# Kernel optimization log

Measured on AMD Instinct MI355X. Metric: run time of the kernel, lower is better.

Reference implementation:

```python
import jax, jax.numpy as jnp
import numpy as np

N_FEATURES = 128
N_ACTIONS = 16
HIDDEN = 256
BATCH = 4096
IN_DIM = N_FEATURES + N_ACTIONS  # 144


def setup_inputs() -> dict:
    key = jax.random.key(0)
    k1, k2, k3, k4 = jax.random.split(key, 4)
    f_t = jax.random.normal(k1, (BATCH, N_FEATURES), dtype=jnp.float32)
    a_t = jax.random.normal(k2, (BATCH, N_ACTIONS), dtype=jnp.float32)
    # Stacked per-feature MLP params (one small MLP per output feature).
    W1 = jax.random.normal(k3, (N_FEATURES, IN_DIM, HIDDEN), dtype=jnp.float32) / np.sqrt(IN_DIM)
    b1 = jnp.zeros((N_FEATURES, HIDDEN), dtype=jnp.float32)
    W2 = jax.random.normal(k4, (N_FEATURES, HIDDEN), dtype=jnp.float32) / np.sqrt(HIDDEN)
    b2 = jnp.zeros((N_FEATURES,), dtype=jnp.float32)
    return {"f_t": f_t, "a_t": a_t, "W1": W1, "b1": b1, "W2": W2, "b2": b2}


def reference(f_t, a_t, W1, b1, W2, b2):
    # fa_t: [B, F+A] shared input to all per-feature models
    fa_t = jnp.concatenate((f_t, a_t), axis=1)
    # Grouped GEMM replacing parallel_apply over n_features tiny MLPs:
    # h: [M, B, H]
    h = jax.nn.relu(jnp.einsum('bi,mih->mbh', fa_t, W1) + b1[:, None, :])
    # out: [B, M]  (each model emits a single scalar per example)
    out = jnp.einsum('mbh,mh->bm', h, W2) + b2[None, :]
    # skip_connection=True, additional=False, all=False -> add f_t
    return out + f_t
```

## Files before the change

### kernel.cpp

```cpp
#include <hip/hip_runtime.h>
#include <hip/hip_bf16.h>

#define BATCH   4096
#define NF      128
#define NA      16
#define IN_DIM  144
#define KP      160
#define KF      192
#define HID     256

typedef __attribute__((ext_vector_type(8))) short bf16x8;
typedef __attribute__((ext_vector_type(4))) float f32x4;
typedef unsigned int u32;

__device__ __forceinline__ void gl_lds16(const void* gsrc, void* ldst) {
    __builtin_amdgcn_global_load_lds(
        (const __attribute__((address_space(1))) u32*)gsrc,
        (__attribute__((address_space(3))) u32*)ldst, 16, 0, 0);
}

__global__ void convert_all(const float* __restrict__ W1,
                            const float* __restrict__ b1,
                            const float* __restrict__ f_t,
                            const float* __restrict__ a_t,
                            __hip_bfloat16* __restrict__ w1t,
                            __hip_bfloat16* __restrict__ fab) {
    const int bid = blockIdx.x;
    const int t = threadIdx.x;
    if (bid < 1280) {
        __shared__ float tile[16][HID];
        int m = bid / 10;
        int kc = bid - m * 10;
        int k0 = kc * 16;
        if (kc < 9) {
#pragma unroll
            for (int i = 0; i < 16; ++i)
                tile[i][t] = W1[((size_t)m * IN_DIM + (k0 + i)) * HID + t];
            __syncthreads();
            union { ushort us[16]; uint4 q[2]; } pk;
#pragma unroll
            for (int i = 0; i < 16; ++i) {
                __hip_bfloat16 h = __float2bfloat16(tile[i][t]);
                pk.us[i] = *(ushort*)&h;
            }
            uint4* dst = (uint4*)(w1t + ((size_t)m * HID + t) * KP + k0);
            dst[0] = pk.q[0];
            dst[1] = pk.q[1];
        } else {
            union { ushort us[8]; uint4 q; } pk;
#pragma unroll
            for (int j = 0; j < 8; ++j) pk.us[j] = 0;
            __hip_bfloat16 hb = __float2bfloat16(b1[(size_t)m * HID + t]);
            pk.us[0] = *(ushort*)&hb;
            uint4 z = {0u, 0u, 0u, 0u};
            uint4* dst = (uint4*)(w1t + ((size_t)m * HID + t) * KP + IN_DIM);
            dst[0] = pk.q;
            dst[1] = z;
        }
    } else {
        int c = (bid - 1280) * 256 + t;
        const int total = BATCH * (KF / 8);
        if (c >= total) return;
        int row = c / 24;
        int cc = c - row * 24;
        union { ushort us[8]; uint4 q; } pk;
#pragma unroll
        for (int j = 0; j < 8; ++j) {
            int k = cc * 8 + j;
            float v;
            if (k < NF)            v = f_t[(size_t)row * NF + k];
            else if (k < IN_DIM)   v = a_t[(size_t)row * NA + (k - NF)];
            else if (k == IN_DIM)  v = 1.0f;
            else                   v = 0.0f;
            __hip_bfloat16 h = __float2bfloat16(v);
            pk.us[j] = *(ushort*)&h;
        }
        int pc = cc ^ (row & 7);
        *(uint4*)(fab + (size_t)row * KF + pc * 8) = pk.q;
    }
}

__global__ __launch_bounds__(256, 3) void fused_mlp(
        const __hip_bfloat16* __restrict__ fab,
        const __hip_bfloat16* __restrict__ w1t,
        const float* __restrict__ W2,
        const float* __restrict__ b2,
        const float* __restrict__ f_t,
        float* __restrict__ out) {
    __shared__ __align__(16) __hip_bfloat16 Abuf[2][32 * KF];
    __shared__ __align__(16) float partial[2][4][32];

    const int bid = blockIdx.x;
    const int m     = bid & 127;
    const int slice = bid >> 7;
    const int row_base = slice * 512;
    const int t = threadIdx.x;
    const int w = t >> 6;
    const int lane = t & 63;
    const int lrow = lane & 15;
    const int g = lane >> 4;
    const int xr = (lrow & 7) << 4;

    bf16x8 bfrag[4][5];
#pragma unroll
    for (int hi = 0; hi < 4; ++hi) {
        const int col = w * 64 + hi * 16 + lrow;
        const __hip_bfloat16* wp = w1t + ((size_t)m * HID + col) * KP + g * 8;
#pragma unroll
        for (int ks = 0; ks < 5; ++ks)
            bfrag[hi][ks] = *(const bf16x8*)(wp + ks * 32);
    }
    f32x4 w2v[4];
#pragma unroll
    for (int hi = 0; hi < 4; ++hi)
        w2v[hi] = *(const f32x4*)(W2 + (size_t)m * HID + w * 64 + hi * 16 + g * 4);
    const float b2v = b2[m];
    const f32x4 zc = (f32x4){0.f, 0.f, 0.f, 0.f};

    {
        const char* src = (const char*)(fab + (size_t)row_base * KF);
        char* dst = (char*)&Abuf[0][0];
#pragma unroll
        for (int i = 0; i < 3; ++i)
            gl_lds16(src + (size_t)(t + i * 256) * 16, dst + (t + i * 256) * 16);
    }
    __syncthreads();

    for (int tile = 0; tile < 16; ++tile) {
        const int cur = tile & 1;
        const int r0 = row_base + tile * 32;

        if (tile < 15) {
            const char* src = (const char*)(fab + (size_t)(r0 + 32) * KF);
            char* dst = (char*)&Abuf[cur ^ 1][0];
#pragma unroll
            for (int i = 0; i < 3; ++i)
                gl_lds16(src + (size_t)(t + i * 256) * 16, dst + (t + i * 256) * 16);
        }
        float skipv = 0.0f;
        if (t < 32) skipv = f_t[(size_t)(r0 + t) * NF + m];

        f32x4 acc[4][2];
        const char* ab = (const char*)&Abuf[cur][0];

        {
            bf16x8 a[2];
#pragma unroll
            for (int bj = 0; bj < 2; ++bj) {
                int off = (bj * 16 + lrow) * 384 + ((g * 16) ^ xr);
                a[bj] = *(const bf16x8*)(ab + off);
            }
#pragma unroll
            for (int hi = 0; hi < 4; ++hi)
#pragma unroll
                for (int bj = 0; bj < 2; ++bj)
                    acc[hi][bj] = __builtin_amdgcn_mfma_f32_16x16x32_bf16(
                        bfrag[hi][0], a[bj], zc, 0, 0, 0);
        }
#pragma unroll
        for (int ks = 1; ks < 5; ++ks) {
            bf16x8 a[2];
#pragma unroll
            for (int bj = 0; bj < 2; ++bj) {
                int off = (bj * 16 + lrow) * 384 + ((ks * 64 + g * 16) ^ xr);
                a[bj] = *(const bf16x8*)(ab + off);
            }
#pragma unroll
            for (int hi = 0; hi < 4; ++hi)
#pragma unroll
                for (int bj = 0; bj < 2; ++bj)
                    acc[hi][bj] = __builtin_amdgcn_mfma_f32_16x16x32_bf16(
                        bfrag[hi][ks], a[bj], acc[hi][bj], 0, 0, 0);
        }

        float sarr[2];
#pragma unroll
        for (int bj = 0; bj < 2; ++bj) {
            float sr0 = 0.f, sr1 = 0.f, sr2 = 0.f, sr3 = 0.f;
#pragma unroll
            for (int hi = 0; hi < 4; ++hi) {
                float h0 = acc[hi][bj][0]; h0 = h0 > 0.f ? h0 : 0.f;
                float h1 = acc[hi][bj][1]; h1 = h1 > 0.f ? h1 : 0.f;
                float h2 = acc[hi][bj][2]; h2 = h2 > 0.f ? h2 : 0.f;
                float h3 = acc[hi][bj][3]; h3 = h3 > 0.f ? h3 : 0.f;
                sr0 = fmaf(h0, w2v[hi][0], sr0);
                sr1 = fmaf(h1, w2v[hi][1], sr1);
                sr2 = fmaf(h2, w2v[hi][2], sr2);
                sr3 = fmaf(h3, w2v[hi][3], sr3);
            }
            float s = (sr0 + sr1) + (sr2 + sr3);
            s += __shfl_xor(s, 16, 64);
            s += __shfl_xor(s, 32, 64);
            sarr[bj] = s;
        }
        if (g < 2)
            partial[cur][w][(g & 1) * 16 + lrow] = (g & 1) ? sarr[1] : sarr[0];

        __syncthreads();
        if (t < 32) {
            float v = (partial[cur][0][t] + partial[cur][1][t])
                    + (partial[cur][2][t] + partial[cur][3][t])
                    + b2v + skipv;
            out[(size_t)(r0 + t) * NF + m] = v;
        }
    }
}

extern "C" void kernel_launch(void* const* d_in, const int* in_sizes, int n_in,
                              void* d_out, int out_size, void* d_ws, size_t ws_size,
                              hipStream_t stream) {
    const float* f_t = (const float*)d_in[0];
    const float* a_t = (const float*)d_in[1];
    const float* W1  = (const float*)d_in[2];
    const float* b1  = (const float*)d_in[3];
    const float* W2  = (const float*)d_in[4];
    const float* b2  = (const float*)d_in[5];
    float* out = (float*)d_out;

    __hip_bfloat16* w1t = (__hip_bfloat16*)d_ws;
    __hip_bfloat16* fab = (__hip_bfloat16*)((char*)d_ws + (size_t)NF * HID * KP * 2);

    hipLaunchKernelGGL(convert_all, dim3(1664), dim3(256), 0, stream,
                       W1, b1, f_t, a_t, w1t, fab);
    hipLaunchKernelGGL(fused_mlp, dim3(1024), dim3(256), 0, stream,
                       fab, w1t, W2, b2, f_t, out);
}
```

Before: 61.06 us.

## Triple-buffer A tiles with two-ahead prefetch and deferred epilogue reduction

Moves the activation tile pipeline from double to triple buffering, prefetching two tiles ahead. Only waves 1-3 issue the global-to-LDS loads, and they wait with a partial vmcnt so one tile of loads stays in flight across the barrier. The per-tile partial-sum reduction and output store move to wave 0 at the start of the next iteration, so each tile needs one barrier instead of two. This costs extra LDS, which may lower occupancy, and relies on hand-written waitcnt/barrier assembly that must match the load counts exactly.

```diff
diff --git a/kernel.cpp b/kernel.cpp
--- a/kernel.cpp
+++ b/kernel.cpp
@@ -87,7 +87,7 @@
         const float* __restrict__ b2,
         const float* __restrict__ f_t,
         float* __restrict__ out) {
-    __shared__ __align__(16) __hip_bfloat16 Abuf[2][32 * KF];
+    __shared__ __align__(16) __hip_bfloat16 Abuf[3][32 * KF];
     __shared__ __align__(16) float partial[2][4][32];
 
     const int bid = blockIdx.x;
@@ -117,28 +117,57 @@
     const float b2v = b2[m];
     const f32x4 zc = (f32x4){0.f, 0.f, 0.f, 0.f};
 
-    {
-        const char* src = (const char*)(fab + (size_t)row_base * KF);
-        char* dst = (char*)&Abuf[0][0];
-#pragma unroll
-        for (int i = 0; i < 3; ++i)
-            gl_lds16(src + (size_t)(t + i * 256) * 16, dst + (t + i * 256) * 16);
-    }
-    __syncthreads();
-
+    if (w >= 1) {
+#pragma unroll
+        for (int tt = 0; tt < 2; ++tt) {
+            const char* src = (const char*)(fab + (size_t)(row_base + tt * 32) * KF);
+            char* dst = (char*)&Abuf[tt][0];
+#pragma unroll
+            for (int i = 0; i < 4; ++i) {
+                int chunk = (w - 1) * 256 + i * 64 + lane;
+                gl_lds16(src + (size_t)chunk * 16, dst + chunk * 16);
+            }
+        }
+    }
+
+    float skip_prev = 0.0f;
     for (int tile = 0; tile < 16; ++tile) {
-        const int cur = tile & 1;
+        const int cur = tile % 3;
         const int r0 = row_base + tile * 32;
 
-        if (tile < 15) {
-            const char* src = (const char*)(fab + (size_t)(r0 + 32) * KF);
-            char* dst = (char*)&Abuf[cur ^ 1][0];
-#pragma unroll
-            for (int i = 0; i < 3; ++i)
-                gl_lds16(src + (size_t)(t + i * 256) * 16, dst + (t + i * 256) * 16);
-        }
-        float skipv = 0.0f;
-        if (t < 32) skipv = f_t[(size_t)(r0 + t) * NF + m];
+        if (w >= 1) {
+            if (tile < 15)
+                asm volatile("s_waitcnt vmcnt(4) lgkmcnt(0)\n\ts_barrier" ::: "memory");
+            else
+                asm volatile("s_waitcnt vmcnt(0) lgkmcnt(0)\n\ts_barrier" ::: "memory");
+        } else {
+            asm volatile("s_waitcnt lgkmcnt(0)\n\ts_barrier" ::: "memory");
+        }
+
+        if (w >= 1 && tile < 14) {
+            const char* src = (const char*)(fab + (size_t)(r0 + 64) * KF);
+            char* dst = (char*)&Abuf[(tile + 2) % 3][0];
+#pragma unroll
+            for (int i = 0; i < 4; ++i) {
+                int chunk = (w - 1) * 256 + i * 64 + lane;
+                gl_lds16(src + (size_t)chunk * 16, dst + chunk * 16);
+            }
+        }
+
+        float skip_cur = 0.0f;
+        if (w == 0) {
+            if (lane < 32) {
+                if (tile >= 1) {
+                    const int pb = (tile - 1) & 1;
+                    float v = (partial[pb][0][lane] + partial[pb][1][lane])
+                            + (partial[pb][2][lane] + partial[pb][3][lane])
+                            + b2v + skip_prev;
+                    out[(size_t)(r0 - 32 + lane) * NF + m] = v;
+                }
+                skip_cur = f_t[(size_t)(r0 + lane) * NF + m];
+            }
+        }
+        skip_prev = skip_cur;
 
         f32x4 acc[4][2];
         const char* ab = (const char*)&Abuf[cur][0];
@@ -194,15 +223,16 @@
             sarr[bj] = s;
         }
         if (g < 2)
-            partial[cur][w][(g & 1) * 16 + lrow] = (g & 1) ? sarr[1] : sarr[0];
-
-        __syncthreads();
-        if (t < 32) {
-            float v = (partial[cur][0][t] + partial[cur][1][t])
-                    + (partial[cur][2][t] + partial[cur][3][t])
-                    + b2v + skipv;
-            out[(size_t)(r0 + t) * NF + m] = v;
-        }
+            partial[tile & 1][w][(g & 1) * 16 + lrow] = (g & 1) ? sarr[1] : sarr[0];
+    }
+
+    asm volatile("s_waitcnt lgkmcnt(0)\n\ts_barrier" ::: "memory");
+    if (w == 0 && lane < 32) {
+        const int pb = 15 & 1;
+        float v = (partial[pb][0][lane] + partial[pb][1][lane])
+                + (partial[pb][2][lane] + partial[pb][3][lane])
+                + b2v + skip_prev;
+        out[(size_t)(row_base + 15 * 32 + lane) * NF + m] = v;
     }
 }
 
```

After: 65.10 us. +6.6%, slower.
